# Kernel optimization log

Hardware: AMD Instinct MI355X
Metric: run time of the kernel (lower is better)

## Reference

```python
import jax, jax.numpy as jnp
import numpy as np
import math

SIZE = 4096

def setup_inputs() -> dict:
    key = jax.random.key(0)
    k_x, k_t = jax.random.split(key)
    x = jax.random.normal(k_x, (4, 2048, SIZE), dtype=jnp.float32)
    # twiddle_factors[0]: the only layer actually used by the original forward
    twiddle = jax.random.normal(k_t, (SIZE // 2, 2, 2), dtype=jnp.float32) / math.sqrt(2.0)
    return {"x": x, "twiddle": twiddle}

def reference(x, twiddle):
    # Original builds a block-diagonal weight W with 2x2 blocks T_k on the
    # diagonal, then computes y = x @ W.T. Equivalently, for each adjacent
    # pair (x[2k], x[2k+1]): y_pair = T_k @ x_pair.
    n = x.shape[-1]
    xp = x.reshape(*x.shape[:-1], n // 2, 2)          # [..., n/2, 2]
    y = jnp.einsum('kab,...kb->...ka', twiddle, xp)    # 2x2 block matvec
    return y.reshape(x.shape)
```

## Files before the change

### kernel.cpp

```cpp
#include <hip/hip_runtime.h>


__global__ __launch_bounds__(256) void butterfly_kernel(
    const float4* __restrict__ x,
    const float4* __restrict__ tw,
    float4* __restrict__ y,
    int n4,
    int row4_mask)
{
    int i = blockIdx.x * blockDim.x + threadIdx.x;
    if (i >= n4) return;

    int p = i & row4_mask;
    float4 xv = x[i];
    float4 t0 = tw[2 * p];
    float4 t1 = tw[2 * p + 1];

    float4 yv;
    yv.x = t0.x * xv.x + t0.y * xv.y;
    yv.y = t0.z * xv.x + t0.w * xv.y;
    yv.z = t1.x * xv.z + t1.y * xv.w;
    yv.w = t1.z * xv.z + t1.w * xv.w;

    y[i] = yv;
}

extern "C" void kernel_launch(void* const* d_in, const int* in_sizes, int n_in,
                              void* d_out, int out_size, void* d_ws, size_t ws_size,
                              hipStream_t stream) {
    const float4* x  = (const float4*)d_in[0];
    const float4* tw = (const float4*)d_in[1];
    float4* y = (float4*)d_out;

    int n4 = out_size / 4;
    int row4_mask = (4096 / 4) - 1;

    dim3 block(256);
    dim3 grid((n4 + 255) / 256);
    butterfly_kernel<<<grid, block, 0, stream>>>(x, tw, y, n4, row4_mask);
}
```

Before: 223.0 us.

## Reuse twiddle registers across 16 rows per block and use nontemporal loads/stores

Switches to a 2D grid where each thread keeps its twiddle factors in registers and processes 16 rows of the same column group, so twiddle loads are amortized across rows. Input and output accesses use nontemporal load/store builtins to avoid polluting cache with streaming data. The grid shrinks 16x, which reduces block-scheduling overhead but also reduces parallelism. It assumes the row count is divisible by 16 and that the row length is fixed at 4096.

```diff
diff --git a/kernel.cpp b/kernel.cpp
--- a/kernel.cpp
+++ b/kernel.cpp
@@ -1,41 +1,47 @@
 #include <hip/hip_runtime.h>
 
 
+typedef float f4 __attribute__((ext_vector_type(4)));
+
+#define ROW4 1024
+#define ROWS_PER_BLOCK 16
+
 __global__ __launch_bounds__(256) void butterfly_kernel(
-    const float4* __restrict__ x,
-    const float4* __restrict__ tw,
-    float4* __restrict__ y,
-    int n4,
-    int row4_mask)
+    const f4* __restrict__ x,
+    const f4* __restrict__ tw,
+    f4* __restrict__ y)
 {
-    int i = blockIdx.x * blockDim.x + threadIdx.x;
-    if (i >= n4) return;
+    const int p  = blockIdx.x * 256 + threadIdx.x;
+    const int r0 = blockIdx.y * ROWS_PER_BLOCK;
 
-    int p = i & row4_mask;
-    float4 xv = x[i];
-    float4 t0 = tw[2 * p];
-    float4 t1 = tw[2 * p + 1];
+    const f4 t0 = tw[2 * p];
+    const f4 t1 = tw[2 * p + 1];
 
-    float4 yv;
-    yv.x = t0.x * xv.x + t0.y * xv.y;
-    yv.y = t0.z * xv.x + t0.w * xv.y;
-    yv.z = t1.x * xv.z + t1.y * xv.w;
-    yv.w = t1.z * xv.z + t1.w * xv.w;
+    const f4* xp = x + (size_t)r0 * ROW4 + p;
+    f4*       yp = y + (size_t)r0 * ROW4 + p;
 
-    y[i] = yv;
+#pragma unroll 4
+    for (int r = 0; r < ROWS_PER_BLOCK; ++r) {
+        f4 xv = __builtin_nontemporal_load(xp + (size_t)r * ROW4);
+        f4 yv;
+        yv.x = t0.x * xv.x + t0.y * xv.y;
+        yv.y = t0.z * xv.x + t0.w * xv.y;
+        yv.z = t1.x * xv.z + t1.y * xv.w;
+        yv.w = t1.z * xv.z + t1.w * xv.w;
+        __builtin_nontemporal_store(yv, yp + (size_t)r * ROW4);
+    }
 }
 
 extern "C" void kernel_launch(void* const* d_in, const int* in_sizes, int n_in,
                               void* d_out, int out_size, void* d_ws, size_t ws_size,
                               hipStream_t stream) {
-    const float4* x  = (const float4*)d_in[0];
-    const float4* tw = (const float4*)d_in[1];
-    float4* y = (float4*)d_out;
+    const f4* x  = (const f4*)d_in[0];
+    const f4* tw = (const f4*)d_in[1];
+    f4* y = (f4*)d_out;
 
-    int n4 = out_size / 4;
-    int row4_mask = (4096 / 4) - 1;
+    const int n_rows = out_size / 4096;
 
     dim3 block(256);
-    dim3 grid((n4 + 255) / 256);
-    butterfly_kernel<<<grid, block, 0, stream>>>(x, tw, y, n4, row4_mask);
+    dim3 grid(ROW4 / 256, n_rows / ROWS_PER_BLOCK);
+    butterfly_kernel<<<grid, block, 0, stream>>>(x, tw, y);
 }
```

Result: slower. 228.4 us (+2.4%).
